# Kernel optimization log

Measured on AMD Instinct MI355X. Metric: run time of the kernel, lower is better.

Reference implementation:

```python
import jax, jax.numpy as jnp
import numpy as np

B, S, D = 4, 1024, 2048
H, G = 16, 2            # num_heads, num_groups (GQA)
HD = D // H             # head_dim = 128


def rotate_half(x):
    x1, x2 = x[..., : x.shape[-1] // 2], x[..., x.shape[-1] // 2 :]
    return jnp.concatenate([-x2, x1], axis=-1)


def setup_inputs() -> dict:
    key = jax.random.key(0)
    ks = jax.random.split(key, 9)
    scale = 0.02
    return {
        "x": jax.random.normal(ks[0], (B, S, D), jnp.float32),
        "wq": jax.random.normal(ks[1], (D, D), jnp.float32) * scale,
        "bq": jnp.zeros((D,), jnp.float32),
        "wk": jax.random.normal(ks[2], (D, G * HD), jnp.float32) * scale,
        "bk": jnp.zeros((G * HD,), jnp.float32),
        "wv": jax.random.normal(ks[3], (D, G * HD), jnp.float32) * scale,
        "bv": jnp.zeros((G * HD,), jnp.float32),
        "wo": jax.random.normal(ks[4], (D, D), jnp.float32) * scale,
        "bo": jnp.zeros((D,), jnp.float32),
    }


def reference(x, wq, bq, wk, bk, wv, bv, wo, bo):
    b, s, d = x.shape
    hd = HD
    # projections (flax Linear: y = x @ kernel + bias)
    q = (x @ wq + bq).reshape(b, s, H, hd)
    k = (x @ wk + bk).reshape(b, s, G, hd)
    v = (x @ wv + bv).reshape(b, s, G, hd)

    # RoPE tables (positions = arange(s), matching q_pos/kv_pos defaults)
    inv_freq = 1.0 / 10000 ** (jnp.arange(0, hd, 2, dtype=jnp.float32) / hd)
    t = jnp.arange(s, dtype=jnp.float32)
    freqs = jnp.outer(t, inv_freq)              # [s, hd/2]
    freqs = jnp.concatenate([freqs, freqs], -1)  # [s, hd]
    sin = jnp.sin(freqs)[:, None, :]             # [s, 1, hd]
    cos = jnp.cos(freqs)[:, None, :]

    q = q * cos + rotate_half(q) * sin
    q = q * (hd ** -0.5)  # module's explicit scale
    k = k * cos + rotate_half(k) * sin

    # GQA: expand K/V groups to full heads (repeats = H // G)
    reps = H // G
    k_exp = jnp.repeat(k, reps, axis=2)  # [b, s, H, hd]
    v_exp = jnp.repeat(v, reps, axis=2)

    # jax.nn.dot_product_attention also applies 1/sqrt(hd) by default,
    # so net scaling is hd**-1 (faithful to the original module).
    scores = jnp.einsum("bqhd,bkhd->bhqk", q, k_exp) * (hd ** -0.5)
    attn = jax.nn.softmax(scores, axis=-1)
    out = jnp.einsum("bhqk,bkhd->bqhd", attn, v_exp).reshape(b, s, d)
    return out @ wo + bo
```

## Files before the change

kernel.cpp:

```cpp
#include <hip/hip_runtime.h>
#include <hip/hip_bf16.h>
#include <type_traits>

typedef __attribute__((ext_vector_type(8))) __bf16 bf16x8;
typedef __attribute__((ext_vector_type(4))) float floatx4;

__device__ inline floatx4 mfma_bf16(bf16x8 a, bf16x8 b, floatx4 c) {
    return __builtin_amdgcn_mfma_f32_16x16x32_bf16(a, b, c, 0, 0, 0);
}

__device__ inline void g2l16(const __hip_bfloat16* g, __hip_bfloat16* l) {
    __builtin_amdgcn_global_load_lds(
        (const __attribute__((address_space(1))) void*)g,
        (__attribute__((address_space(3))) void*)l, 16, 0, 0);
}

__global__ void cast_f32_bf16_k(const float* __restrict__ in,
                                __hip_bfloat16* __restrict__ out, int n4) {
    int i = blockIdx.x * blockDim.x + threadIdx.x;
    if (i < n4) {
        float4 v = ((const float4*)in)[i];
        ushort4 u;
        __hip_bfloat16 a0 = __float2bfloat16(v.x), a1 = __float2bfloat16(v.y);
        __hip_bfloat16 a2 = __float2bfloat16(v.z), a3 = __float2bfloat16(v.w);
        u.x = *(unsigned short*)&a0; u.y = *(unsigned short*)&a1;
        u.z = *(unsigned short*)&a2; u.w = *(unsigned short*)&a3;
        ((ushort4*)out)[i] = u;
    }
}

__global__ void prep_k(const float* __restrict__ wq, const float* __restrict__ wk,
                       const float* __restrict__ wv, const float* __restrict__ wo,
                       const float* __restrict__ bq, const float* __restrict__ bk,
                       const float* __restrict__ bv,
                       __hip_bfloat16* __restrict__ wqkvt,
                       __hip_bfloat16* __restrict__ wot,
                       float* __restrict__ bqkv) {
    int bid = blockIdx.x;
    if (bid >= 9216) {
        int i = (bid - 9216) * 256 + threadIdx.x;
        if (i < 2560)
            bqkv[i] = (i < 2048) ? bq[i] : (i < 2304 ? bk[i - 2048] : bv[i - 2304]);
        return;
    }
    const float* W; __hip_bfloat16* Wt; int C, row_off, cb, rb;
    if (bid < 4096)      { W = wq; Wt = wqkvt; C = 2048; row_off = 0;
                           cb = bid & 63; rb = bid >> 6; }
    else if (bid < 4608) { W = wk; Wt = wqkvt; C = 256;  row_off = 2048;
                           int id = bid - 4096; cb = id & 7; rb = id >> 3; }
    else if (bid < 5120) { W = wv; Wt = wqkvt; C = 256;  row_off = 2304;
                           int id = bid - 4608; cb = id & 7; rb = id >> 3; }
    else                 { W = wo; Wt = wot;   C = 2048; row_off = 0;
                           int id = bid - 5120; cb = id & 63; rb = id >> 6; }
    __shared__ float tile[32][33];
    int c0 = cb * 32, r0 = rb * 32;
    int tx = threadIdx.x & 31, ty0 = threadIdx.x >> 5;
#pragma unroll
    for (int i = 0; i < 4; i++) {
        int ty = ty0 + i * 8;
        tile[ty][tx] = W[(size_t)(r0 + ty) * C + c0 + tx];
    }
    __syncthreads();
#pragma unroll
    for (int i = 0; i < 4; i++) {
        int ty = ty0 + i * 8;
        Wt[(size_t)(row_off + c0 + ty) * 2048 + r0 + tx] = __float2bfloat16(tile[tx][ty]);
    }
}

__global__ __launch_bounds__(256) void gemm_qkv_k(
    const __hip_bfloat16* __restrict__ A,
    const __hip_bfloat16* __restrict__ Bt,
    const float* __restrict__ bias,
    __hip_bfloat16* __restrict__ Qb,
    __hip_bfloat16* __restrict__ Kb,
    __hip_bfloat16* __restrict__ Vlin) {
    __shared__ alignas(16) __hip_bfloat16 As[128 * 32];
    __shared__ alignas(16) __hip_bfloat16 Bs[128 * 32];
    const int t = threadIdx.x, lane = t & 63, w = t >> 6;
    const int quad = lane >> 4, l16 = lane & 15;
    const int bm = blockIdx.y, bn = blockIdx.x;
    const int r_ = t >> 2;
    const int kc_ = (t & 3) ^ ((t >> 3) & 3);
    const int swz = (l16 >> 1) & 3;

    const __hip_bfloat16* gA = A + (size_t)(bm * 128 + r_) * 2048 + kc_ * 8;
    const __hip_bfloat16* gB = Bt + (size_t)(bn * 128 + r_) * 2048 + kc_ * 8;

    floatx4 acc[2][8] = {};

    for (int kt = 0; kt < 2048; kt += 32) {
        g2l16(gA + kt, As + t * 8);
        g2l16(gA + kt + 64 * 2048, As + (t + 256) * 8);
        g2l16(gB + kt, Bs + t * 8);
        g2l16(gB + kt + 64 * 2048, Bs + (t + 256) * 8);
        __syncthreads();
        bf16x8 af[2], bfr[8];
#pragma unroll
        for (int mi = 0; mi < 2; mi++)
            af[mi] = *(const bf16x8*)(As + (w * 32 + mi * 16 + l16) * 32 + (quad ^ swz) * 8);
#pragma unroll
        for (int ni = 0; ni < 8; ni++)
            bfr[ni] = *(const bf16x8*)(Bs + (ni * 16 + l16) * 32 + (quad ^ swz) * 8);
#pragma unroll
        for (int mi = 0; mi < 2; mi++)
#pragma unroll
            for (int ni = 0; ni < 8; ni++)
                acc[mi][ni] = mfma_bf16(af[mi], bfr[ni], acc[mi][ni]);
        __syncthreads();
    }

    const int row_base = bm * 128 + w * 32 + quad * 4;
    if (bn < 18) {
        const float scale = (bn < 16) ? 0.0078125f : 1.0f;
        __hip_bfloat16* dst = (bn < 16) ? Qb : Kb;
        const int nh = (bn < 16) ? 16 : 2;
        const int hh = (bn < 16) ? bn : (bn - 16);
#pragma unroll
        for (int ni = 0; ni < 4; ni++) {
            int j = ni * 16 + l16;
            float invf = __expf(-(float)j * (9.210340371976184f / 64.f));
            float bj  = bias[bn * 128 + j];
            float bj2 = bias[bn * 128 + j + 64];
#pragma unroll
            for (int mi = 0; mi < 2; mi++)
#pragma unroll
                for (int r = 0; r < 4; r++) {
                    int row = row_base + mi * 16 + r;
                    int b = row >> 10, s = row & 1023;
                    float vj  = acc[mi][ni][r] + bj;
                    float vj2 = acc[mi][ni + 4][r] + bj2;
                    float sn, cs;
                    __sincosf((float)s * invf, &sn, &cs);
                    __hip_bfloat16* op = dst + ((size_t)(b * nh + hh) * 1024 + s) * 128;
                    op[j]      = __float2bfloat16((vj * cs - vj2 * sn) * scale);
                    op[j + 64] = __float2bfloat16((vj2 * cs + vj * sn) * scale);
                }
        }
    } else {
        int g = bn - 18;
#pragma unroll
        for (int ni = 0; ni < 8; ni++) {
            int col = ni * 16 + l16;
            float bv = bias[bn * 128 + col];
#pragma unroll
            for (int mi = 0; mi < 2; mi++)
#pragma unroll
                for (int r = 0; r < 4; r++) {
                    int row = row_base + mi * 16 + r;
                    Vlin[(size_t)row * 256 + g * 128 + col] =
                        __float2bfloat16(acc[mi][ni][r] + bv);
                }
        }
    }
}

template <typename OUT_T>
__global__ __launch_bounds__(256) void gemm_bt_k(
    const __hip_bfloat16* __restrict__ A,
    const __hip_bfloat16* __restrict__ Bt,
    const float* __restrict__ bias,
    OUT_T* __restrict__ C,
    int M, int N, int K) {
    __shared__ alignas(16) __hip_bfloat16 As[128 * 32];
    __shared__ alignas(16) __hip_bfloat16 Bs[128 * 32];
    const int t = threadIdx.x;
    const int lane = t & 63;
    const int w = t >> 6;
    const int wm = w & 1, wn = w >> 1;
    const int quad = lane >> 4, l16 = lane & 15;
    const int bm = blockIdx.y, bn = blockIdx.x;
    const int r_ = t >> 2;
    const int kc_ = (t & 3) ^ ((t >> 3) & 3);
    const int swz = (l16 >> 1) & 3;

    const __hip_bfloat16* gA = A + (size_t)(bm * 128 + r_) * K + kc_ * 8;
    const __hip_bfloat16* gB = Bt + (size_t)(bn * 128 + r_) * K + kc_ * 8;

    floatx4 acc[4][4] = {};

    for (int kt = 0; kt < K; kt += 32) {
        g2l16(gA + kt, As + t * 8);
        g2l16(gA + kt + (size_t)64 * K, As + (t + 256) * 8);
        g2l16(gB + kt, Bs + t * 8);
        g2l16(gB + kt + (size_t)64 * K, Bs + (t + 256) * 8);
        __syncthreads();
        bf16x8 af[4], bfr[4];
#pragma unroll
        for (int mi = 0; mi < 4; mi++)
            af[mi] = *(const bf16x8*)(As + (wm * 64 + mi * 16 + l16) * 32 + (quad ^ swz) * 8);
#pragma unroll
        for (int ni = 0; ni < 4; ni++)
            bfr[ni] = *(const bf16x8*)(Bs + (wn * 64 + ni * 16 + l16) * 32 + (quad ^ swz) * 8);
#pragma unroll
        for (int mi = 0; mi < 4; mi++)
#pragma unroll
            for (int ni = 0; ni < 4; ni++)
                acc[mi][ni] = mfma_bf16(af[mi], bfr[ni], acc[mi][ni]);
        __syncthreads();
    }

#pragma unroll
    for (int mi = 0; mi < 4; mi++) {
        int row0 = bm * 128 + wm * 64 + mi * 16 + quad * 4;
#pragma unroll
        for (int ni = 0; ni < 4; ni++) {
            int col = bn * 128 + wn * 64 + ni * 16 + l16;
            float bv = bias[col];
#pragma unroll
            for (int r = 0; r < 4; r++) {
                float v = acc[mi][ni][r] + bv;
                if constexpr (std::is_same<OUT_T, float>::value)
                    C[(size_t)(row0 + r) * N + col] = v;
                else
                    C[(size_t)(row0 + r) * N + col] = __float2bfloat16(v);
            }
        }
    }
}

__global__ void transpose_v_k(const __hip_bfloat16* __restrict__ Vlin,
                              __hip_bfloat16* __restrict__ VT) {
    __shared__ __hip_bfloat16 tile[32][33];
    int bg = blockIdx.z;
    int b = bg >> 1, g = bg & 1;
    int s0 = blockIdx.y * 32, d0 = blockIdx.x * 32;
    int tx = threadIdx.x & 31, ty0 = threadIdx.x >> 5;
#pragma unroll
    for (int i = 0; i < 4; i++) {
        int ty = ty0 + i * 8;
        tile[ty][tx] = Vlin[(size_t)(b * 1024 + s0 + ty) * 256 + g * 128 + d0 + tx];
    }
    __syncthreads();
#pragma unroll
    for (int i = 0; i < 4; i++) {
        int ty = ty0 + i * 8;
        VT[((size_t)(b * 2 + g) * 128 + d0 + ty) * 1024 + s0 + tx] = tile[tx][ty];
    }
}

__global__ __launch_bounds__(256, 2) void attn_k(
    const __hip_bfloat16* __restrict__ Qb,
    const __hip_bfloat16* __restrict__ Kb,
    const __hip_bfloat16* __restrict__ VT,
    __hip_bfloat16* __restrict__ AO) {
    constexpr int PLD = 72;
    __shared__ alignas(16) __hip_bfloat16 Ks[64 * 128];
    __shared__ alignas(16) __hip_bfloat16 Vs[128 * 64];
    __shared__ alignas(16) __hip_bfloat16 Ps[4][32 * PLD];

    const int bh = blockIdx.x;
    const int b = bh >> 4, h = bh & 15, g = h >> 3;
    const int t = threadIdx.x, lane = t & 63, w = t >> 6;
    const int quad = lane >> 4, l16 = lane & 15;
    const int q0 = blockIdx.y * 128 + w * 32;

    const __hip_bfloat16* Qp = Qb + ((size_t)bh * 1024 + q0 + l16) * 128 + quad * 8;
    bf16x8 aq[2][4];
#pragma unroll
    for (int mi = 0; mi < 2; mi++)
#pragma unroll
        for (int kc = 0; kc < 4; kc++)
            aq[mi][kc] = *(const bf16x8*)(Qp + mi * 16 * 128 + kc * 32);

    const int bg = b * 2 + g;
    const __hip_bfloat16* Kstage = Kb + (size_t)bg * 1024 * 128
        + (t >> 4) * 128 + ((t & 15) ^ (t >> 4)) * 8;
    const __hip_bfloat16* Vstage = VT + (size_t)bg * 128 * 1024
        + (t >> 3) * 1024 + ((t & 7) ^ ((t >> 3) & 7)) * 8;

    float l_part[2][4] = {};
    floatx4 o[2][8] = {};

    for (int kv = 0; kv < 1024; kv += 64) {
#pragma unroll
        for (int j = 0; j < 4; j++)
            g2l16(Kstage + (size_t)(kv + j * 16) * 128, Ks + (j * 256 + t) * 8);
#pragma unroll
        for (int j = 0; j < 4; j++)
            g2l16(Vstage + (size_t)j * 32 * 1024 + kv, Vs + (j * 256 + t) * 8);
        __syncthreads();

        floatx4 s[2][4] = {};
#pragma unroll
        for (int nj = 0; nj < 4; nj++)
#pragma unroll
            for (int kc = 0; kc < 4; kc++) {
                bf16x8 kb = *(const bf16x8*)(Ks + (nj * 16 + l16) * 128
                                             + (((kc * 4 + quad) ^ l16) * 8));
                s[0][nj] = mfma_bf16(aq[0][kc], kb, s[0][nj]);
                s[1][nj] = mfma_bf16(aq[1][kc], kb, s[1][nj]);
            }

        __hip_bfloat16* pl = Ps[w];
#pragma unroll
        for (int mi = 0; mi < 2; mi++)
#pragma unroll
            for (int nj = 0; nj < 4; nj++)
#pragma unroll
                for (int r = 0; r < 4; r++) {
                    float p = __expf(s[mi][nj][r]);
                    l_part[mi][r] += p;
                    pl[(mi * 16 + quad * 4 + r) * PLD + nj * 16 + l16] =
                        __float2bfloat16(p);
                }
        asm volatile("s_waitcnt lgkmcnt(0)" ::: "memory");

        bf16x8 ap[2][2];
#pragma unroll
        for (int mi = 0; mi < 2; mi++)
#pragma unroll
            for (int kc2 = 0; kc2 < 2; kc2++)
                ap[mi][kc2] = *(const bf16x8*)(pl + (mi * 16 + l16) * PLD
                                               + kc2 * 32 + quad * 8);

#pragma unroll
        for (int ni = 0; ni < 8; ni++)
#pragma unroll
            for (int kc2 = 0; kc2 < 2; kc2++) {
                bf16x8 vb = *(const bf16x8*)(Vs + (ni * 16 + l16) * 64
                                             + (((kc2 * 4 + quad) ^ (l16 & 7)) * 8));
                o[0][ni] = mfma_bf16(ap[0][kc2], vb, o[0][ni]);
                o[1][ni] = mfma_bf16(ap[1][kc2], vb, o[1][ni]);
            }
        __syncthreads();
    }

#pragma unroll
    for (int mi = 0; mi < 2; mi++)
#pragma unroll
        for (int r = 0; r < 4; r++) {
            float sum = l_part[mi][r];
            sum += __shfl_xor(sum, 1);
            sum += __shfl_xor(sum, 2);
            sum += __shfl_xor(sum, 4);
            sum += __shfl_xor(sum, 8);
            float inv = 1.f / sum;
            size_t srow = (size_t)b * 1024 + q0 + mi * 16 + quad * 4 + r;
#pragma unroll
            for (int ni = 0; ni < 8; ni++)
                AO[srow * 2048 + h * 128 + ni * 16 + l16] =
                    __float2bfloat16(o[mi][ni][r] * inv);
        }
}

extern "C" void kernel_launch(void* const* d_in, const int* in_sizes, int n_in,
                              void* d_out, int out_size, void* d_ws, size_t ws_size,
                              hipStream_t stream) {
    (void)in_sizes; (void)n_in; (void)out_size; (void)ws_size;
    const float* x  = (const float*)d_in[0];
    const float* wq = (const float*)d_in[1];
    const float* bq = (const float*)d_in[2];
    const float* wk = (const float*)d_in[3];
    const float* bk = (const float*)d_in[4];
    const float* wv = (const float*)d_in[5];
    const float* bv = (const float*)d_in[6];
    const float* wo = (const float*)d_in[7];
    const float* bo = (const float*)d_in[8];
    float* out = (float*)d_out;

    char* ws = (char*)d_ws;
    __hip_bfloat16* xb    = (__hip_bfloat16*)(ws + 0);
    __hip_bfloat16* AO    = xb;
    __hip_bfloat16* wqkvt = (__hip_bfloat16*)(ws + 16777216);
    __hip_bfloat16* wot   = (__hip_bfloat16*)(ws + 27262976);
    __hip_bfloat16* Qb    = (__hip_bfloat16*)(ws + 35651584);
    __hip_bfloat16* Kb    = (__hip_bfloat16*)(ws + 52428800);
    __hip_bfloat16* Vlin  = (__hip_bfloat16*)(ws + 54525952);
    __hip_bfloat16* VT    = (__hip_bfloat16*)(ws + 56623104);
    float*          bqkv  = (float*)(ws + 58720256);

    cast_f32_bf16_k<<<8192, 256, 0, stream>>>(x, xb, 2097152);
    prep_k<<<9226, 256, 0, stream>>>(wq, wk, wv, wo, bq, bk, bv, wqkvt, wot, bqkv);
    gemm_qkv_k<<<dim3(20, 32), 256, 0, stream>>>(xb, wqkvt, bqkv, Qb, Kb, Vlin);
    transpose_v_k<<<dim3(4, 32, 8), 256, 0, stream>>>(Vlin, VT);
    attn_k<<<dim3(64, 8), 256, 0, stream>>>(Qb, Kb, VT, AO);
    gemm_bt_k<float><<<dim3(16, 32), 256, 0, stream>>>(AO, wot, bo, out, 4096, 2048, 2048);
}
```

Before: 280.1 us.

## Rewrite QKV GEMM with 256x256 tiles and 4-stage async LDS pipeline

The fused QKV projection GEMM moves from 128x128 tiles with 256 threads and a single LDS buffer to 256x256 tiles with 512 threads. It uses a 4-slot ring of global-to-LDS loads with explicit vmcnt waits, so loads run three k-steps ahead, and raises wave priority around the MFMA block. The epilogue is reorganised so each Q tile covers two heads, one tile holds both K groups, and one holds V. The aim is to hide memory latency and cut global traffic per FLOP. In exchange the grid shrinks to 160 blocks with about 128KB LDS each, which may leave many CUs idle.

```diff
diff --git a/kernel.cpp b/kernel.cpp
--- a/kernel.cpp
+++ b/kernel.cpp
@@ -68,88 +68,116 @@
     }
 }
 
-__global__ __launch_bounds__(256) void gemm_qkv_k(
+__global__ __launch_bounds__(512, 2) void gemm_qkv_k(
     const __hip_bfloat16* __restrict__ A,
     const __hip_bfloat16* __restrict__ Bt,
     const float* __restrict__ bias,
     __hip_bfloat16* __restrict__ Qb,
     __hip_bfloat16* __restrict__ Kb,
     __hip_bfloat16* __restrict__ Vlin) {
-    __shared__ alignas(16) __hip_bfloat16 As[128 * 32];
-    __shared__ alignas(16) __hip_bfloat16 Bs[128 * 32];
+    __shared__ alignas(16) __hip_bfloat16 As[4][256 * 32];
+    __shared__ alignas(16) __hip_bfloat16 Bs[4][256 * 32];
     const int t = threadIdx.x, lane = t & 63, w = t >> 6;
     const int quad = lane >> 4, l16 = lane & 15;
+    const int wm = w >> 2, wn = w & 3;
     const int bm = blockIdx.y, bn = blockIdx.x;
-    const int r_ = t >> 2;
-    const int kc_ = (t & 3) ^ ((t >> 3) & 3);
+
+    const int r0 = t >> 2;
+    const int sc = (t & 3) ^ ((t >> 3) & 3);
+    const __hip_bfloat16* gA = A + (size_t)(bm * 256 + r0) * 2048 + sc * 8;
+    const __hip_bfloat16* gB = Bt + (size_t)(bn * 256 + r0) * 2048 + sc * 8;
+
     const int swz = (l16 >> 1) & 3;
-
-    const __hip_bfloat16* gA = A + (size_t)(bm * 128 + r_) * 2048 + kc_ * 8;
-    const __hip_bfloat16* gB = Bt + (size_t)(bn * 128 + r_) * 2048 + kc_ * 8;
-
-    floatx4 acc[2][8] = {};
-
-    for (int kt = 0; kt < 2048; kt += 32) {
-        g2l16(gA + kt, As + t * 8);
-        g2l16(gA + kt + 64 * 2048, As + (t + 256) * 8);
-        g2l16(gB + kt, Bs + t * 8);
-        g2l16(gB + kt + 64 * 2048, Bs + (t + 256) * 8);
-        __syncthreads();
-        bf16x8 af[2], bfr[8];
-#pragma unroll
-        for (int mi = 0; mi < 2; mi++)
-            af[mi] = *(const bf16x8*)(As + (w * 32 + mi * 16 + l16) * 32 + (quad ^ swz) * 8);
-#pragma unroll
-        for (int ni = 0; ni < 8; ni++)
-            bfr[ni] = *(const bf16x8*)(Bs + (ni * 16 + l16) * 32 + (quad ^ swz) * 8);
-#pragma unroll
-        for (int mi = 0; mi < 2; mi++)
-#pragma unroll
-            for (int ni = 0; ni < 8; ni++)
-                acc[mi][ni] = mfma_bf16(af[mi], bfr[ni], acc[mi][ni]);
-        __syncthreads();
-    }
-
-    const int row_base = bm * 128 + w * 32 + quad * 4;
-    if (bn < 18) {
-        const float scale = (bn < 16) ? 0.0078125f : 1.0f;
-        __hip_bfloat16* dst = (bn < 16) ? Qb : Kb;
-        const int nh = (bn < 16) ? 16 : 2;
-        const int hh = (bn < 16) ? bn : (bn - 16);
-#pragma unroll
-        for (int ni = 0; ni < 4; ni++) {
-            int j = ni * 16 + l16;
-            float invf = __expf(-(float)j * (9.210340371976184f / 64.f));
-            float bj  = bias[bn * 128 + j];
-            float bj2 = bias[bn * 128 + j + 64];
-#pragma unroll
-            for (int mi = 0; mi < 2; mi++)
-#pragma unroll
-                for (int r = 0; r < 4; r++) {
-                    int row = row_base + mi * 16 + r;
-                    int b = row >> 10, s = row & 1023;
-                    float vj  = acc[mi][ni][r] + bj;
-                    float vj2 = acc[mi][ni + 4][r] + bj2;
-                    float sn, cs;
-                    __sincosf((float)s * invf, &sn, &cs);
-                    __hip_bfloat16* op = dst + ((size_t)(b * nh + hh) * 1024 + s) * 128;
+    const int aoff = (wm * 128 + l16) * 32 + (quad ^ swz) * 8;
+    const int boff = (wn * 16 + l16) * 32 + (quad ^ swz) * 8;
+
+    floatx4 acc[8][4] = {};
+
+#define STAGE_U(u) do { \
+        int sl_ = (u) & 3; \
+        g2l16(gA + (size_t)(u) * 32,              As[sl_] + t * 8); \
+        g2l16(gA + (size_t)(u) * 32 + 128 * 2048, As[sl_] + (512 + t) * 8); \
+        g2l16(gB + (size_t)(u) * 32,              Bs[sl_] + t * 8); \
+        g2l16(gB + (size_t)(u) * 32 + 128 * 2048, Bs[sl_] + (512 + t) * 8); \
+    } while (0)
+
+    STAGE_U(0); STAGE_U(1); STAGE_U(2);
+    asm volatile("s_waitcnt vmcnt(8)" ::: "memory");
+    __builtin_amdgcn_s_barrier();
+
+#define PHASE_U(u, DOSTAGE, VMSTR) do { \
+        if (DOSTAGE) STAGE_U((u) + 3); \
+        const __hip_bfloat16* pA_ = As[(u) & 3] + aoff; \
+        const __hip_bfloat16* pB_ = Bs[(u) & 3] + boff; \
+        bf16x8 afr[8], bfr[4]; \
+        _Pragma("unroll") for (int rb_ = 0; rb_ < 8; ++rb_) \
+            afr[rb_] = *(const bf16x8*)(pA_ + rb_ * 512); \
+        _Pragma("unroll") for (int cb_ = 0; cb_ < 4; ++cb_) \
+            bfr[cb_] = *(const bf16x8*)(pB_ + cb_ * 2048); \
+        asm volatile("s_waitcnt " VMSTR ::: "memory");  \
+        __builtin_amdgcn_s_barrier(); \
+        __builtin_amdgcn_s_setprio(1); \
+        _Pragma("unroll") for (int rb_ = 0; rb_ < 8; ++rb_) \
+            _Pragma("unroll") for (int cb_ = 0; cb_ < 4; ++cb_) \
+                acc[rb_][cb_] = mfma_bf16(afr[rb_], bfr[cb_], acc[rb_][cb_]); \
+        __builtin_amdgcn_s_setprio(0); \
+        __builtin_amdgcn_s_barrier(); \
+    } while (0)
+
+    for (int u = 0; u < 61; ++u)
+        PHASE_U(u, true, "vmcnt(8)");
+    PHASE_U(61, false, "vmcnt(4)");
+    PHASE_U(62, false, "vmcnt(0)");
+    PHASE_U(63, false, "vmcnt(0)");
+#undef PHASE_U
+#undef STAGE_U
+
+    const int row_hi = bm * 256 + wm * 128 + quad * 4;
+    if (bn < 9) {
+        const float scale = (bn < 8) ? 0.0078125f : 1.0f;
+        __hip_bfloat16* dst = (bn < 8) ? Qb : Kb;
+        const int nh = (bn < 8) ? 16 : 2;
+        const int hbase = (bn < 8) ? bn * 2 : 0;
+        const int j = wn * 16 + l16;
+        const float invf = __expf(-(float)j * (9.210340371976184f / 64.f));
+        const float b0 = bias[bn * 256 + j];
+        const float b1 = bias[bn * 256 + j + 64];
+        const float b2 = bias[bn * 256 + 128 + j];
+        const float b3 = bias[bn * 256 + 128 + j + 64];
+#pragma unroll
+        for (int rb = 0; rb < 8; ++rb)
+#pragma unroll
+            for (int r = 0; r < 4; ++r) {
+                int row = row_hi + rb * 16 + r;
+                int b = row >> 10, s = row & 1023;
+                float sn, cs;
+                __sincosf((float)s * invf, &sn, &cs);
+                {
+                    float vj = acc[rb][0][r] + b0, vj2 = acc[rb][1][r] + b1;
+                    __hip_bfloat16* op =
+                        dst + ((size_t)(b * nh + hbase) * 1024 + s) * 128;
                     op[j]      = __float2bfloat16((vj * cs - vj2 * sn) * scale);
                     op[j + 64] = __float2bfloat16((vj2 * cs + vj * sn) * scale);
                 }
-        }
+                {
+                    float vj = acc[rb][2][r] + b2, vj2 = acc[rb][3][r] + b3;
+                    __hip_bfloat16* op =
+                        dst + ((size_t)(b * nh + hbase + 1) * 1024 + s) * 128;
+                    op[j]      = __float2bfloat16((vj * cs - vj2 * sn) * scale);
+                    op[j + 64] = __float2bfloat16((vj2 * cs + vj * sn) * scale);
+                }
+            }
     } else {
-        int g = bn - 18;
-#pragma unroll
-        for (int ni = 0; ni < 8; ni++) {
-            int col = ni * 16 + l16;
-            float bv = bias[bn * 128 + col];
-#pragma unroll
-            for (int mi = 0; mi < 2; mi++)
-#pragma unroll
-                for (int r = 0; r < 4; r++) {
-                    int row = row_base + mi * 16 + r;
-                    Vlin[(size_t)row * 256 + g * 128 + col] =
-                        __float2bfloat16(acc[mi][ni][r] + bv);
+#pragma unroll
+        for (int cb = 0; cb < 4; ++cb) {
+            int c = cb * 64 + wn * 16 + l16;
+            float bv = bias[2304 + c];
+#pragma unroll
+            for (int rb = 0; rb < 8; ++rb)
+#pragma unroll
+                for (int r = 0; r < 4; ++r) {
+                    int row = row_hi + rb * 16 + r;
+                    Vlin[(size_t)row * 256 + c] = __float2bfloat16(acc[rb][cb][r] + bv);
                 }
         }
     }
@@ -372,7 +400,7 @@
 
     cast_f32_bf16_k<<<8192, 256, 0, stream>>>(x, xb, 2097152);
     prep_k<<<9226, 256, 0, stream>>>(wq, wk, wv, wo, bq, bk, bv, wqkvt, wot, bqkv);
-    gemm_qkv_k<<<dim3(20, 32), 256, 0, stream>>>(xb, wqkvt, bqkv, Qb, Kb, Vlin);
+    gemm_qkv_k<<<dim3(10, 16), 512, 0, stream>>>(xb, wqkvt, bqkv, Qb, Kb, Vlin);
     transpose_v_k<<<dim3(4, 32, 8), 256, 0, stream>>>(Vlin, VT);
     attn_k<<<dim3(64, 8), 256, 0, stream>>>(Qb, Kb, VT, AO);
     gemm_bt_k<float><<<dim3(16, 32), 256, 0, stream>>>(AO, wot, bo, out, 4096, 2048, 2048);
```

Measured after the change: 308.3 us. 1.1x slower.

## Add four-stage LDS prefetch pipeline to QKV and output projection GEMMs

Applied to the files above, without the earlier changes.

Both bf16 GEMM kernels now use four LDS buffers for the A and B tiles instead of one. Each block prefetches three k-tiles ahead with async global-to-LDS loads, waits on explicit vmcnt counts, and uses raw barriers with s_setprio around the MFMA block. The goal is to overlap global memory latency with matrix-core work rather than stalling on a full sync every k-step. In exchange, LDS per block grows to 64 KB, which can lower occupancy, and correctness now depends on the hand-tuned waitcnt and barrier ordering.

```diff
diff --git a/kernel.cpp b/kernel.cpp
--- a/kernel.cpp
+++ b/kernel.cpp
@@ -75,8 +75,8 @@
     __hip_bfloat16* __restrict__ Qb,
     __hip_bfloat16* __restrict__ Kb,
     __hip_bfloat16* __restrict__ Vlin) {
-    __shared__ alignas(16) __hip_bfloat16 As[128 * 32];
-    __shared__ alignas(16) __hip_bfloat16 Bs[128 * 32];
+    __shared__ alignas(16) __hip_bfloat16 As[4][128 * 32];
+    __shared__ alignas(16) __hip_bfloat16 Bs[4][128 * 32];
     const int t = threadIdx.x, lane = t & 63, w = t >> 6;
     const int quad = lane >> 4, l16 = lane & 15;
     const int bm = blockIdx.y, bn = blockIdx.x;
@@ -89,26 +89,46 @@
 
     floatx4 acc[2][8] = {};
 
-    for (int kt = 0; kt < 2048; kt += 32) {
-        g2l16(gA + kt, As + t * 8);
-        g2l16(gA + kt + 64 * 2048, As + (t + 256) * 8);
-        g2l16(gB + kt, Bs + t * 8);
-        g2l16(gB + kt + 64 * 2048, Bs + (t + 256) * 8);
-        __syncthreads();
-        bf16x8 af[2], bfr[8];
-#pragma unroll
-        for (int mi = 0; mi < 2; mi++)
-            af[mi] = *(const bf16x8*)(As + (w * 32 + mi * 16 + l16) * 32 + (quad ^ swz) * 8);
-#pragma unroll
-        for (int ni = 0; ni < 8; ni++)
-            bfr[ni] = *(const bf16x8*)(Bs + (ni * 16 + l16) * 32 + (quad ^ swz) * 8);
-#pragma unroll
-        for (int mi = 0; mi < 2; mi++)
-#pragma unroll
-            for (int ni = 0; ni < 8; ni++)
-                acc[mi][ni] = mfma_bf16(af[mi], bfr[ni], acc[mi][ni]);
-        __syncthreads();
-    }
+#define STAGE_U(u) do { \
+        int sl_ = (u) & 3; \
+        g2l16(gA + (u) * 32,             As[sl_] + t * 8); \
+        g2l16(gA + (u) * 32 + 64 * 2048, As[sl_] + (t + 256) * 8); \
+        g2l16(gB + (u) * 32,             Bs[sl_] + t * 8); \
+        g2l16(gB + (u) * 32 + 64 * 2048, Bs[sl_] + (t + 256) * 8); \
+    } while (0)
+
+    STAGE_U(0); STAGE_U(1); STAGE_U(2);
+    asm volatile("s_waitcnt vmcnt(8)" ::: "memory");
+    __builtin_amdgcn_s_barrier();
+
+#define PHASE_U(u, DOSTAGE, VMSTR) do { \
+        if (DOSTAGE) STAGE_U((u) + 3); \
+        const __hip_bfloat16* pA_ = As[(u) & 3]; \
+        const __hip_bfloat16* pB_ = Bs[(u) & 3]; \
+        bf16x8 af_[2], bf_[8]; \
+        _Pragma("unroll") for (int mi_ = 0; mi_ < 2; ++mi_) \
+            af_[mi_] = *(const bf16x8*)(pA_ + (w * 32 + mi_ * 16 + l16) * 32 \
+                                        + (quad ^ swz) * 8); \
+        _Pragma("unroll") for (int ni_ = 0; ni_ < 8; ++ni_) \
+            bf_[ni_] = *(const bf16x8*)(pB_ + (ni_ * 16 + l16) * 32 \
+                                        + (quad ^ swz) * 8); \
+        asm volatile("s_waitcnt " VMSTR ::: "memory");  \
+        __builtin_amdgcn_s_barrier(); \
+        __builtin_amdgcn_s_setprio(1); \
+        _Pragma("unroll") for (int mi_ = 0; mi_ < 2; ++mi_) \
+            _Pragma("unroll") for (int ni_ = 0; ni_ < 8; ++ni_) \
+                acc[mi_][ni_] = mfma_bf16(af_[mi_], bf_[ni_], acc[mi_][ni_]); \
+        __builtin_amdgcn_s_setprio(0); \
+        __builtin_amdgcn_s_barrier(); \
+    } while (0)
+
+    for (int u = 0; u < 61; ++u)
+        PHASE_U(u, true, "vmcnt(8)");
+    PHASE_U(61, false, "vmcnt(4)");
+    PHASE_U(62, false, "vmcnt(0)");
+    PHASE_U(63, false, "vmcnt(0)");
+#undef PHASE_U
+#undef STAGE_U
 
     const int row_base = bm * 128 + w * 32 + quad * 4;
     if (bn < 18) {
@@ -162,8 +182,8 @@
     const float* __restrict__ bias,
     OUT_T* __restrict__ C,
     int M, int N, int K) {
-    __shared__ alignas(16) __hip_bfloat16 As[128 * 32];
-    __shared__ alignas(16) __hip_bfloat16 Bs[128 * 32];
+    __shared__ alignas(16) __hip_bfloat16 As[4][128 * 32];
+    __shared__ alignas(16) __hip_bfloat16 Bs[4][128 * 32];
     const int t = threadIdx.x;
     const int lane = t & 63;
     const int w = t >> 6;
@@ -179,26 +199,47 @@
 
     floatx4 acc[4][4] = {};
 
-    for (int kt = 0; kt < K; kt += 32) {
-        g2l16(gA + kt, As + t * 8);
-        g2l16(gA + kt + (size_t)64 * K, As + (t + 256) * 8);
-        g2l16(gB + kt, Bs + t * 8);
-        g2l16(gB + kt + (size_t)64 * K, Bs + (t + 256) * 8);
-        __syncthreads();
-        bf16x8 af[4], bfr[4];
-#pragma unroll
-        for (int mi = 0; mi < 4; mi++)
-            af[mi] = *(const bf16x8*)(As + (wm * 64 + mi * 16 + l16) * 32 + (quad ^ swz) * 8);
-#pragma unroll
-        for (int ni = 0; ni < 4; ni++)
-            bfr[ni] = *(const bf16x8*)(Bs + (wn * 64 + ni * 16 + l16) * 32 + (quad ^ swz) * 8);
-#pragma unroll
-        for (int mi = 0; mi < 4; mi++)
-#pragma unroll
-            for (int ni = 0; ni < 4; ni++)
-                acc[mi][ni] = mfma_bf16(af[mi], bfr[ni], acc[mi][ni]);
-        __syncthreads();
-    }
+#define STAGE_U(u) do { \
+        int sl_ = (u) & 3; \
+        g2l16(gA + (size_t)(u) * 32,            As[sl_] + t * 8); \
+        g2l16(gA + (size_t)(u) * 32 + 64 * K,   As[sl_] + (t + 256) * 8); \
+        g2l16(gB + (size_t)(u) * 32,            Bs[sl_] + t * 8); \
+        g2l16(gB + (size_t)(u) * 32 + 64 * K,   Bs[sl_] + (t + 256) * 8); \
+    } while (0)
+
+    const int nu = K >> 5;
+    STAGE_U(0); STAGE_U(1); STAGE_U(2);
+    asm volatile("s_waitcnt vmcnt(8)" ::: "memory");
+    __builtin_amdgcn_s_barrier();
+
+#define PHASE_U(u, DOSTAGE, VMSTR) do { \
+        if (DOSTAGE) STAGE_U((u) + 3); \
+        const __hip_bfloat16* pA_ = As[(u) & 3]; \
+        const __hip_bfloat16* pB_ = Bs[(u) & 3]; \
+        bf16x8 af_[4], bf_[4]; \
+        _Pragma("unroll") for (int mi_ = 0; mi_ < 4; ++mi_) \
+            af_[mi_] = *(const bf16x8*)(pA_ + (wm * 64 + mi_ * 16 + l16) * 32 \
+                                        + (quad ^ swz) * 8); \
+        _Pragma("unroll") for (int ni_ = 0; ni_ < 4; ++ni_) \
+            bf_[ni_] = *(const bf16x8*)(pB_ + (wn * 64 + ni_ * 16 + l16) * 32 \
+                                        + (quad ^ swz) * 8); \
+        asm volatile("s_waitcnt " VMSTR ::: "memory"); \
+        __builtin_amdgcn_s_barrier(); \
+        __builtin_amdgcn_s_setprio(1); \
+        _Pragma("unroll") for (int mi_ = 0; mi_ < 4; ++mi_) \
+            _Pragma("unroll") for (int ni_ = 0; ni_ < 4; ++ni_) \
+                acc[mi_][ni_] = mfma_bf16(af_[mi_], bf_[ni_], acc[mi_][ni_]); \
+        __builtin_amdgcn_s_setprio(0); \
+        __builtin_amdgcn_s_barrier(); \
+    } while (0)
+
+    for (int u = 0; u < nu - 3; ++u)
+        PHASE_U(u, true, "vmcnt(8)");
+    PHASE_U(nu - 3, false, "vmcnt(4)");
+    PHASE_U(nu - 2, false, "vmcnt(0)");
+    PHASE_U(nu - 1, false, "vmcnt(0)");
+#undef PHASE_U
+#undef STAGE_U
 
 #pragma unroll
     for (int mi = 0; mi < 4; mi++) {
```

Result: slower. 323.2 us (+15.4%).

## Fuse V transpose into QKV GEMM epilogue and load V fragments directly from global

Applied to the files above, without the earlier changes.

The QKV GEMM epilogue for V tiles now stages results in a padded LDS tile and writes V already transposed into VT, which removes the separate transpose kernel and the Vlin round trip. The attention kernel no longer stages V through LDS. Each lane loads its V MFMA operands straight from global memory into registers. This cuts one launch, LDS traffic and LDS footprint, at the cost of extra LDS (about 34 KB) in the GEMM kernel, which may lower occupancy, and uncoalesced, latency-exposed global loads for V in attention.

```diff
diff --git a/kernel.cpp b/kernel.cpp
--- a/kernel.cpp
+++ b/kernel.cpp
@@ -74,9 +74,10 @@
     const float* __restrict__ bias,
     __hip_bfloat16* __restrict__ Qb,
     __hip_bfloat16* __restrict__ Kb,
-    __hip_bfloat16* __restrict__ Vlin) {
+    __hip_bfloat16* __restrict__ VT) {
     __shared__ alignas(16) __hip_bfloat16 As[128 * 32];
     __shared__ alignas(16) __hip_bfloat16 Bs[128 * 32];
+    __shared__ alignas(16) __hip_bfloat16 vtile[128][136];
     const int t = threadIdx.x, lane = t & 63, w = t >> 6;
     const int quad = lane >> 4, l16 = lane & 15;
     const int bm = blockIdx.y, bn = blockIdx.x;
@@ -138,7 +139,7 @@
                 }
         }
     } else {
-        int g = bn - 18;
+        const int g = bn - 18;
 #pragma unroll
         for (int ni = 0; ni < 8; ni++) {
             int col = ni * 16 + l16;
@@ -147,10 +148,18 @@
             for (int mi = 0; mi < 2; mi++)
 #pragma unroll
                 for (int r = 0; r < 4; r++) {
-                    int row = row_base + mi * 16 + r;
-                    Vlin[(size_t)row * 256 + g * 128 + col] =
-                        __float2bfloat16(acc[mi][ni][r] + bv);
+                    int lr = w * 32 + mi * 16 + quad * 4 + r;
+                    vtile[col][lr] = __float2bfloat16(acc[mi][ni][r] + bv);
                 }
+        }
+        __syncthreads();
+        const int b = bm >> 3, s0 = (bm & 7) * 128;
+        const int dd = t >> 4, sc8 = (t & 15) * 8;
+#pragma unroll
+        for (int pass = 0; pass < 8; pass++) {
+            int d = pass * 16 + dd;
+            bf16x8 v = *(const bf16x8*)&vtile[d][sc8];
+            *(bf16x8*)(VT + ((size_t)((b * 2 + g) * 128 + d)) * 1024 + s0 + sc8) = v;
         }
     }
 }
@@ -219,26 +228,6 @@
     }
 }
 
-__global__ void transpose_v_k(const __hip_bfloat16* __restrict__ Vlin,
-                              __hip_bfloat16* __restrict__ VT) {
-    __shared__ __hip_bfloat16 tile[32][33];
-    int bg = blockIdx.z;
-    int b = bg >> 1, g = bg & 1;
-    int s0 = blockIdx.y * 32, d0 = blockIdx.x * 32;
-    int tx = threadIdx.x & 31, ty0 = threadIdx.x >> 5;
-#pragma unroll
-    for (int i = 0; i < 4; i++) {
-        int ty = ty0 + i * 8;
-        tile[ty][tx] = Vlin[(size_t)(b * 1024 + s0 + ty) * 256 + g * 128 + d0 + tx];
-    }
-    __syncthreads();
-#pragma unroll
-    for (int i = 0; i < 4; i++) {
-        int ty = ty0 + i * 8;
-        VT[((size_t)(b * 2 + g) * 128 + d0 + ty) * 1024 + s0 + tx] = tile[tx][ty];
-    }
-}
-
 __global__ __launch_bounds__(256, 2) void attn_k(
     const __hip_bfloat16* __restrict__ Qb,
     const __hip_bfloat16* __restrict__ Kb,
@@ -246,7 +235,6 @@
     __hip_bfloat16* __restrict__ AO) {
     constexpr int PLD = 72;
     __shared__ alignas(16) __hip_bfloat16 Ks[64 * 128];
-    __shared__ alignas(16) __hip_bfloat16 Vs[128 * 64];
     __shared__ alignas(16) __hip_bfloat16 Ps[4][32 * PLD];
 
     const int bh = blockIdx.x;
@@ -266,8 +254,7 @@
     const int bg = b * 2 + g;
     const __hip_bfloat16* Kstage = Kb + (size_t)bg * 1024 * 128
         + (t >> 4) * 128 + ((t & 15) ^ (t >> 4)) * 8;
-    const __hip_bfloat16* Vstage = VT + (size_t)bg * 128 * 1024
-        + (t >> 3) * 1024 + ((t & 7) ^ ((t >> 3) & 7)) * 8;
+    const __hip_bfloat16* Vg = VT + ((size_t)bg * 128 + l16) * 1024 + quad * 8;
 
     float l_part[2][4] = {};
     floatx4 o[2][8] = {};
@@ -276,9 +263,14 @@
 #pragma unroll
         for (int j = 0; j < 4; j++)
             g2l16(Kstage + (size_t)(kv + j * 16) * 128, Ks + (j * 256 + t) * 8);
-#pragma unroll
-        for (int j = 0; j < 4; j++)
-            g2l16(Vstage + (size_t)j * 32 * 1024 + kv, Vs + (j * 256 + t) * 8);
+
+        bf16x8 vbf[8][2];
+#pragma unroll
+        for (int ni = 0; ni < 8; ni++)
+#pragma unroll
+            for (int kc2 = 0; kc2 < 2; kc2++)
+                vbf[ni][kc2] = *(const bf16x8*)(Vg + (size_t)ni * 16 * 1024
+                                                + kv + kc2 * 32);
         __syncthreads();
 
         floatx4 s[2][4] = {};
@@ -318,10 +310,8 @@
         for (int ni = 0; ni < 8; ni++)
 #pragma unroll
             for (int kc2 = 0; kc2 < 2; kc2++) {
-                bf16x8 vb = *(const bf16x8*)(Vs + (ni * 16 + l16) * 64
-                                             + (((kc2 * 4 + quad) ^ (l16 & 7)) * 8));
-                o[0][ni] = mfma_bf16(ap[0][kc2], vb, o[0][ni]);
-                o[1][ni] = mfma_bf16(ap[1][kc2], vb, o[1][ni]);
+                o[0][ni] = mfma_bf16(ap[0][kc2], vbf[ni][kc2], o[0][ni]);
+                o[1][ni] = mfma_bf16(ap[1][kc2], vbf[ni][kc2], o[1][ni]);
             }
         __syncthreads();
     }
@@ -366,14 +356,12 @@
     __hip_bfloat16* wot   = (__hip_bfloat16*)(ws + 27262976);
     __hip_bfloat16* Qb    = (__hip_bfloat16*)(ws + 35651584);
     __hip_bfloat16* Kb    = (__hip_bfloat16*)(ws + 52428800);
-    __hip_bfloat16* Vlin  = (__hip_bfloat16*)(ws + 54525952);
     __hip_bfloat16* VT    = (__hip_bfloat16*)(ws + 56623104);
     float*          bqkv  = (float*)(ws + 58720256);
 
     cast_f32_bf16_k<<<8192, 256, 0, stream>>>(x, xb, 2097152);
     prep_k<<<9226, 256, 0, stream>>>(wq, wk, wv, wo, bq, bk, bv, wqkvt, wot, bqkv);
-    gemm_qkv_k<<<dim3(20, 32), 256, 0, stream>>>(xb, wqkvt, bqkv, Qb, Kb, Vlin);
-    transpose_v_k<<<dim3(4, 32, 8), 256, 0, stream>>>(Vlin, VT);
+    gemm_qkv_k<<<dim3(20, 32), 256, 0, stream>>>(xb, wqkvt, bqkv, Qb, Kb, VT);
     attn_k<<<dim3(64, 8), 256, 0, stream>>>(Qb, Kb, VT, AO);
     gemm_bt_k<float><<<dim3(16, 32), 256, 0, stream>>>(AO, wot, bo, out, 4096, 2048, 2048);
 }
```

Result: slower. 322.8 us (+15.2%).
